# Kernel optimization log

Hardware: AMD Instinct MI355X
Metric: run time of the kernel (lower is better)

Reference implementation:

```python
import jax, jax.numpy as jnp
import numpy as np

N = 100000       # num_nodes
E = 800000       # num edges (avg degree 8)
EMB = 64         # emb_dim
HID = 256        # hidden_dim


def setup_inputs() -> dict:
    key = jax.random.key(0)
    k1, k2, k3, k4, k5, k6, k7 = jax.random.split(key, 7)
    def xavier(k, fan_in, fan_out):
        limit = float(np.sqrt(6.0 / (fan_in + fan_out)))
        return jax.random.uniform(k, (fan_in, fan_out), jnp.float32, -limit, limit)
    return {
        "row": jax.random.randint(k1, (E,), 0, N, dtype=jnp.int64) if jax.config.jax_enable_x64 else jax.random.randint(k1, (E,), 0, N).astype(jnp.int32),
        "col": jax.random.randint(k2, (E,), 0, N).astype(jnp.int32),
        "val": jax.random.uniform(k3, (E,), jnp.float32),
        "emb": jax.random.normal(k4, (N, EMB), jnp.float32) * 0.02,
        "W0": xavier(k5, EMB, HID),
        "W1": xavier(k6, HID, HID),
        "W2": xavier(k7, HID, HID),
    }


def reference(row, col, val, emb, W0, W1, W2):
    # SpMM: out[r] = sum_{edges e with row[e]==r} val[e] * emb[col[e]]
    msgs = val[:, None] * emb[col]                      # [E, EMB] gather + scale
    x = jax.ops.segment_sum(msgs, row, num_segments=N)  # [N, EMB] scatter-add
    # MLP (bias-free linears; dropout=0.0 / eval mode => identity)
    x = jax.nn.relu(x @ W0)   # [N, HID]
    x = jax.nn.relu(x @ W1)   # [N, HID]
    x = x @ W2                # [N, HID]
    return x
```

## Files before the change

kernel.cpp:

```cpp
#include <hip/hip_runtime.h>
#include <hip/hip_bf16.h>

#define EMB 64
#define HID 256

typedef __attribute__((ext_vector_type(8))) short short8_t;
typedef __attribute__((ext_vector_type(4))) float f32x4;

__device__ __forceinline__ unsigned short f2bf(float f)
{
    union { float f; unsigned int u; } c; c.f = f;
    unsigned int u = c.u;
    u += 0x7fffu + ((u >> 16) & 1u);
    return (unsigned short)(u >> 16);
}
__device__ __forceinline__ float bf2f(unsigned short b)
{
    union { unsigned int u; float f; } c; c.u = ((unsigned int)b) << 16;
    return c.f;
}

__global__ __launch_bounds__(256) void prep_kernel(
    const float* __restrict__ emb, const float* __restrict__ W0,
    const float* __restrict__ W1, const float* __restrict__ W2,
    int* __restrict__ counts, unsigned short* __restrict__ embb,
    unsigned short* __restrict__ W0f, unsigned short* __restrict__ W1f,
    unsigned short* __restrict__ W2f, int M, int zb, int cb)
{
    int b = blockIdx.x;
    if (b < zb) {
        int idx = (b * 256 + threadIdx.x) * 4;
        if (idx + 3 < M) {
            int4 z; z.x = 0; z.y = 0; z.z = 0; z.w = 0;
            *(int4*)&counts[idx] = z;
        } else {
            for (int i = idx; i < M; ++i) counts[i] = 0;
        }
        return;
    }
    b -= zb;
    if (b < cb) {
        int idx = (b * 256 + threadIdx.x) * 4;
        if (idx + 3 < M * EMB) {
            float4 v = *(const float4*)&emb[idx];
            ushort4 o;
            o.x = f2bf(v.x); o.y = f2bf(v.y); o.z = f2bf(v.z); o.w = f2bf(v.w);
            *(ushort4*)&embb[idx] = o;
        }
        return;
    }
    b -= cb;
    if (b < 8) {
        int i    = b * 256 + threadIdx.x;
        int lane = i & 63;
        int kc   = (i >> 6) & 1;
        int nt   = i >> 7;
        int lr   = lane & 15, kg = lane >> 4;
        unsigned short tmp[8];
#pragma unroll
        for (int j = 0; j < 8; ++j)
            tmp[j] = f2bf(W0[(kc * 32 + kg * 8 + j) * HID + nt * 16 + lr]);
        *(short8_t*)&W0f[(size_t)i * 8] = *(short8_t*)tmp;
        return;
    }
    b -= 8;
    if (b < 32) {
        int i    = b * 256 + threadIdx.x;
        int lane = i & 63;
        int kc   = (i >> 6) & 7;
        int nt   = i >> 9;
        int lr   = lane & 15, kg = lane >> 4;
        unsigned short tmp[8];
#pragma unroll
        for (int j = 0; j < 8; ++j)
            tmp[j] = f2bf(W1[(kc * 32 + kg * 8 + j) * HID + nt * 16 + lr]);
        *(short8_t*)&W1f[(size_t)i * 8] = *(short8_t*)tmp;
        return;
    }
    b -= 32;
    {
        int i    = b * 256 + threadIdx.x;
        int lane = i & 63;
        int kc   = (i >> 6) & 7;
        int nt   = i >> 9;
        int lr   = lane & 15, kg = lane >> 4;
        unsigned short tmp[8];
#pragma unroll
        for (int j = 0; j < 8; ++j)
            tmp[j] = f2bf(W2[(kc * 32 + kg * 8 + j) * HID + nt * 16 + lr]);
        *(short8_t*)&W2f[(size_t)i * 8] = *(short8_t*)tmp;
    }
}

__global__ __launch_bounds__(256) void hist_kernel(
    const int* __restrict__ row, int* __restrict__ counts, int E)
{
    int base = (blockIdx.x * 256 + threadIdx.x) * 4;
    if (base + 3 < E) {
        int4 r4 = *(const int4*)&row[base];
        atomicAdd(&counts[r4.x], 1);
        atomicAdd(&counts[r4.y], 1);
        atomicAdd(&counts[r4.z], 1);
        atomicAdd(&counts[r4.w], 1);
    } else {
        for (int i = base; i < E; ++i) atomicAdd(&counts[row[i]], 1);
    }
}

__global__ __launch_bounds__(256) void scan_phase1(
    const int* __restrict__ counts, int* __restrict__ excl,
    int* __restrict__ blockSums, int n)
{
    __shared__ int s[256];
    int t = threadIdx.x;
    int base = blockIdx.x * 1024 + t * 4;
    int4 v = {0, 0, 0, 0};
    if (base + 3 < n) {
        v = *(const int4*)&counts[base];
    } else {
        if (base + 0 < n) v.x = counts[base + 0];
        if (base + 1 < n) v.y = counts[base + 1];
        if (base + 2 < n) v.z = counts[base + 2];
        if (base + 3 < n) v.w = counts[base + 3];
    }
    int tsum = v.x + v.y + v.z + v.w;
    s[t] = tsum;
    __syncthreads();
#pragma unroll
    for (int off = 1; off < 256; off <<= 1) {
        int val = (t >= off) ? s[t - off] : 0;
        __syncthreads();
        s[t] += val;
        __syncthreads();
    }
    if (t == 255) blockSums[blockIdx.x] = s[255];
    int e0 = s[t] - tsum;
    int e1 = e0 + v.x;
    int e2 = e1 + v.y;
    int e3 = e2 + v.z;
    if (base + 0 < n) excl[base + 0] = e0;
    if (base + 1 < n) excl[base + 1] = e1;
    if (base + 2 < n) excl[base + 2] = e2;
    if (base + 3 < n) excl[base + 3] = e3;
}

__global__ __launch_bounds__(256) void scan_phase2(int* blockSums, int nb)
{
    __shared__ int s[256];
    int t = threadIdx.x;
    int v = (t < nb) ? blockSums[t] : 0;
    s[t] = v;
    __syncthreads();
#pragma unroll
    for (int off = 1; off < 256; off <<= 1) {
        int val = (t >= off) ? s[t - off] : 0;
        __syncthreads();
        s[t] += val;
        __syncthreads();
    }
    if (t < nb) blockSums[t] = s[t] - v;
}

__global__ __launch_bounds__(256) void scan_phase3(
    int* __restrict__ offsets, const int* __restrict__ blockSums,
    int* __restrict__ cursor, int n)
{
    int i = blockIdx.x * 256 + threadIdx.x;
    if (i >= n) return;
    int o = offsets[i] + blockSums[i >> 10];
    offsets[i] = o;
    cursor[i]  = o;
}

__global__ __launch_bounds__(256) void scatter_kernel(
    const int* __restrict__ row, const int* __restrict__ col,
    const float* __restrict__ val, int* __restrict__ cursor,
    uint2* __restrict__ edata, int E)
{
    int e = blockIdx.x * 256 + threadIdx.x;
    if (e >= E) return;
    int r = row[e];
    int pos = atomicAdd(&cursor[r], 1);
    uint2 d;
    d.x = (unsigned)col[e];
    d.y = __float_as_uint(val[e]);
    edata[pos] = d;
}

__global__ __launch_bounds__(256) void pull_kernel(
    const int* __restrict__ offsets, const int* __restrict__ counts,
    const uint2* __restrict__ edata, const unsigned short* __restrict__ embb,
    unsigned short* __restrict__ xb, int Nn)
{
    int r    = blockIdx.x * 4 + (threadIdx.x >> 6);
    int lane = threadIdx.x & 63;
    if (r >= Nn) return;
    int beg = offsets[r];
    int cnt = counts[r];
    float acc = 0.f;
    for (int i = 0; i < cnt; i += 8) {
        uint2 ed[8];
#pragma unroll
        for (int j = 0; j < 8; ++j) {
            int idx = i + j;
            idx = (idx < cnt) ? idx : (cnt - 1);
            ed[j] = edata[beg + idx];
        }
        float g[8];
#pragma unroll
        for (int j = 0; j < 8; ++j)
            g[j] = bf2f(embb[(size_t)ed[j].x * EMB + lane]);
#pragma unroll
        for (int j = 0; j < 8; ++j) {
            float v = (i + j < cnt) ? __uint_as_float(ed[j].y) : 0.f;
            acc += v * g[j];
        }
    }
    xb[(size_t)r * EMB + lane] = f2bf(acc);
}

__global__ __launch_bounds__(256) void mlp_fused(
    const unsigned short* __restrict__ xb,
    const unsigned short* __restrict__ W0f,
    const unsigned short* __restrict__ W1f,
    const unsigned short* __restrict__ W2f,
    float* __restrict__ out, int M)
{
    __shared__ unsigned short H[64 * 256];

    const int t    = threadIdx.x;
    const int lane = t & 63;
    const int w    = t >> 6;
    const int lr   = lane & 15;
    const int kg   = lane >> 4;
    const int row0 = blockIdx.x * 64;
    char* Hb = (char*)H;

#define HOFF(row, bytecol) ((((row) * 512) + (bytecol)) ^ (((row) & 7) << 4))

    short8_t ax[2][4];
#pragma unroll
    for (int kc = 0; kc < 2; ++kc)
#pragma unroll
        for (int m = 0; m < 4; ++m) {
            int gr = row0 + m * 16 + lr;
            ax[kc][m] = *(const short8_t*)(xb + (size_t)(gr < M ? gr : 0) * EMB
                                           + kc * 32 + kg * 8);
        }
    f32x4 acc[4][4] = {};
#pragma unroll
    for (int kc = 0; kc < 2; ++kc) {
        short8_t b[4];
#pragma unroll
        for (int n = 0; n < 4; ++n)
            b[n] = *(const short8_t*)&W0f[(size_t)(((w * 4 + n) * 2 + kc) * 64 + lane) * 8];
#pragma unroll
        for (int m = 0; m < 4; ++m)
#pragma unroll
            for (int n = 0; n < 4; ++n)
                acc[m][n] = __builtin_amdgcn_mfma_f32_16x16x32_bf16(
                    ax[kc][m], b[n], acc[m][n], 0, 0, 0);
    }
#pragma unroll
    for (int m = 0; m < 4; ++m)
#pragma unroll
        for (int r = 0; r < 4; ++r)
#pragma unroll
            for (int n = 0; n < 4; ++n)
                *(unsigned short*)(Hb + HOFF(m * 16 + kg * 4 + r,
                                             (w * 64 + n * 16 + lr) * 2)) =
                    f2bf(fmaxf(acc[m][n][r], 0.f));
    __syncthreads();

    f32x4 acc2[4][4] = {};
#pragma unroll
    for (int kc = 0; kc < 8; ++kc) {
        short8_t a[4], b[4];
#pragma unroll
        for (int n = 0; n < 4; ++n)
            b[n] = *(const short8_t*)&W1f[(size_t)(((w * 4 + n) * 8 + kc) * 64 + lane) * 8];
#pragma unroll
        for (int m = 0; m < 4; ++m)
            a[m] = *(const short8_t*)(Hb + HOFF(m * 16 + lr, kc * 64 + kg * 16));
#pragma unroll
        for (int m = 0; m < 4; ++m)
#pragma unroll
            for (int n = 0; n < 4; ++n)
                acc2[m][n] = __builtin_amdgcn_mfma_f32_16x16x32_bf16(
                    a[m], b[n], acc2[m][n], 0, 0, 0);
    }
    __syncthreads();
#pragma unroll
    for (int m = 0; m < 4; ++m)
#pragma unroll
        for (int r = 0; r < 4; ++r)
#pragma unroll
            for (int n = 0; n < 4; ++n)
                *(unsigned short*)(Hb + HOFF(m * 16 + kg * 4 + r,
                                             (w * 64 + n * 16 + lr) * 2)) =
                    f2bf(fmaxf(acc2[m][n][r], 0.f));
    __syncthreads();

    f32x4 acc3[4][4] = {};
#pragma unroll
    for (int kc = 0; kc < 8; ++kc) {
        short8_t a[4], b[4];
#pragma unroll
        for (int n = 0; n < 4; ++n)
            b[n] = *(const short8_t*)&W2f[(size_t)(((w * 4 + n) * 8 + kc) * 64 + lane) * 8];
#pragma unroll
        for (int m = 0; m < 4; ++m)
            a[m] = *(const short8_t*)(Hb + HOFF(m * 16 + lr, kc * 64 + kg * 16));
#pragma unroll
        for (int m = 0; m < 4; ++m)
#pragma unroll
            for (int n = 0; n < 4; ++n)
                acc3[m][n] = __builtin_amdgcn_mfma_f32_16x16x32_bf16(
                    a[m], b[n], acc3[m][n], 0, 0, 0);
    }
#pragma unroll
    for (int m = 0; m < 4; ++m)
#pragma unroll
        for (int r = 0; r < 4; ++r) {
            int gr = row0 + m * 16 + kg * 4 + r;
            if (gr < M)
#pragma unroll
                for (int n = 0; n < 4; ++n)
                    out[(size_t)gr * HID + w * 64 + n * 16 + lr] = acc3[m][n][r];
        }
#undef HOFF
}

__global__ __launch_bounds__(256) void spmm_kernel(
    const int* __restrict__ row, const int* __restrict__ col,
    const float* __restrict__ val, const float* __restrict__ emb,
    float* __restrict__ x, int E)
{
    int gid  = blockIdx.x * blockDim.x + threadIdx.x;
    int e    = gid >> 6;
    int lane = gid & 63;
    if (e >= E) return;
    unsafeAtomicAdd(&x[(size_t)row[e] * EMB + lane],
                    val[e] * emb[(size_t)col[e] * EMB + lane]);
}

template<int K, bool RELU>
__global__ __launch_bounds__(256) void gemm_f32(
    const float* A, const float* __restrict__ B, float* C, int M)
{
    __shared__ float As[64][17];
    __shared__ float Bs[16][256];

    const int t    = threadIdx.x;
    const int tn   = t & 15;
    const int row0 = blockIdx.x * 64;
    const int sk = t & 15;
    const int sm = (t >> 4) * 4;

    float acc[4][16];
#pragma unroll
    for (int i = 0; i < 4; ++i)
#pragma unroll
        for (int j = 0; j < 16; ++j) acc[i][j] = 0.f;

    const int mB = ((t & 63) >> 4) * 4;
    const int wq = t >> 6;
    const int myM = (wq * 16) + mB;

    for (int k0 = 0; k0 < K; k0 += 16) {
        __syncthreads();
#pragma unroll
        for (int i = 0; i < 4; ++i) {
            int m  = sm + i;
            int gr = row0 + m;
            As[m][sk] = (gr < M) ? A[(size_t)gr * K + k0 + sk] : 0.f;
        }
#pragma unroll
        for (int r = 0; r < 16; ++r)
            Bs[r][t] = B[(size_t)(k0 + r) * 256 + t];
        __syncthreads();

#pragma unroll
        for (int kk = 0; kk < 16; ++kk) {
            float a0 = As[myM + 0][kk];
            float a1 = As[myM + 1][kk];
            float a2 = As[myM + 2][kk];
            float a3 = As[myM + 3][kk];
            float4 b[4];
#pragma unroll
            for (int j = 0; j < 4; ++j)
                b[j] = *(const float4*)&Bs[kk][tn * 4 + j * 64];
#pragma unroll
            for (int j = 0; j < 4; ++j) {
                acc[0][j*4+0] += a0 * b[j].x;  acc[0][j*4+1] += a0 * b[j].y;
                acc[0][j*4+2] += a0 * b[j].z;  acc[0][j*4+3] += a0 * b[j].w;
                acc[1][j*4+0] += a1 * b[j].x;  acc[1][j*4+1] += a1 * b[j].y;
                acc[1][j*4+2] += a1 * b[j].z;  acc[1][j*4+3] += a1 * b[j].w;
                acc[2][j*4+0] += a2 * b[j].x;  acc[2][j*4+1] += a2 * b[j].y;
                acc[2][j*4+2] += a2 * b[j].z;  acc[2][j*4+3] += a2 * b[j].w;
                acc[3][j*4+0] += a3 * b[j].x;  acc[3][j*4+1] += a3 * b[j].y;
                acc[3][j*4+2] += a3 * b[j].z;  acc[3][j*4+3] += a3 * b[j].w;
            }
        }
    }

#pragma unroll
    for (int i = 0; i < 4; ++i) {
        int gr = row0 + myM + i;
        if (gr < M) {
#pragma unroll
            for (int j = 0; j < 4; ++j) {
                float4 o;
                o.x = acc[i][j*4+0]; o.y = acc[i][j*4+1];
                o.z = acc[i][j*4+2]; o.w = acc[i][j*4+3];
                if (RELU) {
                    o.x = fmaxf(o.x, 0.f); o.y = fmaxf(o.y, 0.f);
                    o.z = fmaxf(o.z, 0.f); o.w = fmaxf(o.w, 0.f);
                }
                *(float4*)&C[(size_t)gr * 256 + tn * 4 + j * 64] = o;
            }
        }
    }
}

extern "C" void kernel_launch(void* const* d_in, const int* in_sizes, int n_in,
                              void* d_out, int out_size, void* d_ws, size_t ws_size,
                              hipStream_t stream)
{
    const int*   row = (const int*)d_in[0];
    const int*   col = (const int*)d_in[1];
    const float* val = (const float*)d_in[2];
    const float* emb = (const float*)d_in[3];
    const float* W0  = (const float*)d_in[4];
    const float* W1  = (const float*)d_in[5];
    const float* W2  = (const float*)d_in[6];
    float* out = (float*)d_out;

    const int E = in_sizes[0];
    const int M = in_sizes[3] / EMB;

    char* ws = (char*)d_ws;

    size_t off = 0;
    auto alloc = [&](size_t bytes) { size_t o = off; off = (off + bytes + 255) & ~(size_t)255; return o; };
    const size_t off_counts = alloc((size_t)M * 4);
    const size_t off_offs   = alloc((size_t)M * 4);
    const size_t off_cursor = alloc((size_t)M * 4);
    const size_t off_bsums  = alloc(1024);
    const size_t off_edata  = alloc((size_t)E * 8);
    const size_t off_embb   = alloc((size_t)M * EMB * 2);
    const size_t off_xb     = alloc((size_t)M * EMB * 2);
    const size_t off_w0     = alloc((size_t)EMB * HID * 2);
    const size_t off_w1     = alloc((size_t)HID * HID * 2);
    const size_t off_w2     = alloc((size_t)HID * HID * 2);
    const size_t need       = off;

    int gblocks = (M + 63) / 64;

    if (ws_size >= need) {
        int*   counts = (int*)(ws + off_counts);
        int*   offs   = (int*)(ws + off_offs);
        int*   cursor = (int*)(ws + off_cursor);
        int*   bsums  = (int*)(ws + off_bsums);
        uint2* edata  = (uint2*)(ws + off_edata);
        unsigned short* embb = (unsigned short*)(ws + off_embb);
        unsigned short* xb  = (unsigned short*)(ws + off_xb);
        unsigned short* W0f = (unsigned short*)(ws + off_w0);
        unsigned short* W1f = (unsigned short*)(ws + off_w1);
        unsigned short* W2f = (unsigned short*)(ws + off_w2);

        int zb = (M / 4 + 255) / 256;
        int cb = ((M * EMB) / 4 + 255) / 256;
        int prep_blocks = zb + cb + 8 + 32 + 32;
        prep_kernel<<<prep_blocks, 256, 0, stream>>>(
            emb, W0, W1, W2, counts, embb, W0f, W1f, W2f, M, zb, cb);

        hist_kernel<<<(E / 4 + 255) / 256, 256, 0, stream>>>(row, counts, E);
        int nb = (M + 1023) / 1024;
        scan_phase1<<<nb, 256, 0, stream>>>(counts, offs, bsums, M);
        scan_phase2<<<1, 256, 0, stream>>>(bsums, nb);
        scan_phase3<<<(M + 255) / 256, 256, 0, stream>>>(offs, bsums, cursor, M);
        scatter_kernel<<<(E + 255) / 256, 256, 0, stream>>>(row, col, val, cursor, edata, E);

        pull_kernel<<<(M + 3) / 4, 256, 0, stream>>>(offs, counts, edata, embb, xb, M);

        mlp_fused<<<gblocks, 256, 0, stream>>>(xb, W0f, W1f, W2f, out, M);
    } else {
        float* x = (float*)ws;
        (void)hipMemsetAsync(x, 0, (size_t)M * EMB * sizeof(float), stream);
        spmm_kernel<<<(E + 3) / 4, 256, 0, stream>>>(row, col, val, emb, x, E);
        gemm_f32<EMB, true ><<<gblocks, 256, 0, stream>>>(x,   W0, out, M);
        gemm_f32<HID, true ><<<gblocks, 256, 0, stream>>>(out, W1, out, M);
        gemm_f32<HID, false><<<gblocks, 256, 0, stream>>>(out, W2, out, M);
    }
}
```

Baseline: 201.0 us.

## Vectorize scatter, grid-stride pull with prefetch, stage MLP output through LDS

```diff
diff --git a/kernel.cpp b/kernel.cpp
--- a/kernel.cpp
+++ b/kernel.cpp
@@ -177,46 +177,74 @@
     const float* __restrict__ val, int* __restrict__ cursor,
     uint2* __restrict__ edata, int E)
 {
-    int e = blockIdx.x * 256 + threadIdx.x;
-    if (e >= E) return;
-    int r = row[e];
-    int pos = atomicAdd(&cursor[r], 1);
-    uint2 d;
-    d.x = (unsigned)col[e];
-    d.y = __float_as_uint(val[e]);
-    edata[pos] = d;
-}
-
+    int base = (blockIdx.x * 256 + threadIdx.x) * 4;
+    if (base + 3 < E) {
+        int4   r4 = *(const int4*)&row[base];
+        int4   c4 = *(const int4*)&col[base];
+        float4 v4 = *(const float4*)&val[base];
+        int p0 = atomicAdd(&cursor[r4.x], 1);
+        int p1 = atomicAdd(&cursor[r4.y], 1);
+        int p2 = atomicAdd(&cursor[r4.z], 1);
+        int p3 = atomicAdd(&cursor[r4.w], 1);
+        uint2 d;
+        d.x = (unsigned)c4.x; d.y = __float_as_uint(v4.x); edata[p0] = d;
+        d.x = (unsigned)c4.y; d.y = __float_as_uint(v4.y); edata[p1] = d;
+        d.x = (unsigned)c4.z; d.y = __float_as_uint(v4.z); edata[p2] = d;
+        d.x = (unsigned)c4.w; d.y = __float_as_uint(v4.w); edata[p3] = d;
+    } else {
+        for (int e = base; e < E; ++e) {
+            int pos = atomicAdd(&cursor[row[e]], 1);
+            uint2 d;
+            d.x = (unsigned)col[e];
+            d.y = __float_as_uint(val[e]);
+            edata[pos] = d;
+        }
+    }
+}
+
+#define ROWS_PER_WAVE 8
 __global__ __launch_bounds__(256) void pull_kernel(
     const int* __restrict__ offsets, const int* __restrict__ counts,
     const uint2* __restrict__ edata, const unsigned short* __restrict__ embb,
     unsigned short* __restrict__ xb, int Nn)
 {
-    int r    = blockIdx.x * 4 + (threadIdx.x >> 6);
-    int lane = threadIdx.x & 63;
-    if (r >= Nn) return;
-    int beg = offsets[r];
-    int cnt = counts[r];
-    float acc = 0.f;
-    for (int i = 0; i < cnt; i += 8) {
-        uint2 ed[8];
-#pragma unroll
-        for (int j = 0; j < 8; ++j) {
-            int idx = i + j;
-            idx = (idx < cnt) ? idx : (cnt - 1);
-            ed[j] = edata[beg + idx];
-        }
-        float g[8];
-#pragma unroll
-        for (int j = 0; j < 8; ++j)
-            g[j] = bf2f(embb[(size_t)ed[j].x * EMB + lane]);
-#pragma unroll
-        for (int j = 0; j < 8; ++j) {
-            float v = (i + j < cnt) ? __uint_as_float(ed[j].y) : 0.f;
-            acc += v * g[j];
-        }
-    }
-    xb[(size_t)r * EMB + lane] = f2bf(acc);
+    const int nw   = gridDim.x * 4;
+    const int wid  = blockIdx.x * 4 + (threadIdx.x >> 6);
+    const int lane = threadIdx.x & 63;
+    if (wid >= Nn) return;
+
+    int beg = __builtin_amdgcn_readfirstlane(offsets[wid]);
+    int cnt = __builtin_amdgcn_readfirstlane(counts[wid]);
+    for (int r = wid; r < Nn; r += nw) {
+        int rn = r + nw;
+        int begN = 0, cntN = 0;
+        if (rn < Nn) {
+            begN = __builtin_amdgcn_readfirstlane(offsets[rn]);
+            cntN = __builtin_amdgcn_readfirstlane(counts[rn]);
+        }
+
+        float acc = 0.f;
+        for (int i = 0; i < cnt; i += 8) {
+            uint2 ed[8];
+#pragma unroll
+            for (int j = 0; j < 8; ++j) {
+                int idx = i + j;
+                idx = (idx < cnt) ? idx : (cnt - 1);
+                ed[j] = edata[beg + idx];
+            }
+            float g[8];
+#pragma unroll
+            for (int j = 0; j < 8; ++j)
+                g[j] = bf2f(embb[(size_t)ed[j].x * EMB + lane]);
+#pragma unroll
+            for (int j = 0; j < 8; ++j) {
+                float v = (i + j < cnt) ? __uint_as_float(ed[j].y) : 0.f;
+                acc += v * g[j];
+            }
+        }
+        xb[(size_t)r * EMB + lane] = f2bf(acc);
+        beg = begN; cnt = cntN;
+    }
 }
 
 __global__ __launch_bounds__(256) void mlp_fused(
@@ -318,16 +346,26 @@
                 acc3[m][n] = __builtin_amdgcn_mfma_f32_16x16x32_bf16(
                     a[m], b[n], acc3[m][n], 0, 0, 0);
     }
-#pragma unroll
-    for (int m = 0; m < 4; ++m)
-#pragma unroll
-        for (int r = 0; r < 4; ++r) {
-            int gr = row0 + m * 16 + kg * 4 + r;
+    __syncthreads();
+
+    float* Hf = (float*)H;
+    const int ebase = w * 1280;
+#pragma unroll
+    for (int m = 0; m < 4; ++m) {
+#pragma unroll
+        for (int n = 0; n < 4; ++n)
+#pragma unroll
+            for (int r = 0; r < 4; ++r)
+                Hf[ebase + (kg * 4 + r) * 68 + n * 16 + lr] = acc3[m][n][r];
+#pragma unroll
+        for (int p = 0; p < 4; ++p) {
+            int rl = (lane >> 4) + p * 4;
+            f32x4 v = *(const f32x4*)&Hf[ebase + rl * 68 + (lane & 15) * 4];
+            int gr = row0 + m * 16 + rl;
             if (gr < M)
-#pragma unroll
-                for (int n = 0; n < 4; ++n)
-                    out[(size_t)gr * HID + w * 64 + n * 16 + lr] = acc3[m][n][r];
-        }
+                *(f32x4*)&out[(size_t)gr * HID + w * 64 + (lane & 15) * 4] = v;
+        }
+    }
 #undef HOFF
 }
 
@@ -455,8 +493,6 @@
     const size_t off_w2     = alloc((size_t)HID * HID * 2);
     const size_t need       = off;
 
-    int gblocks = (M + 63) / 64;
-
     if (ws_size >= need) {
         int*   counts = (int*)(ws + off_counts);
         int*   offs   = (int*)(ws + off_offs);
@@ -480,15 +516,18 @@
         scan_phase1<<<nb, 256, 0, stream>>>(counts, offs, bsums, M);
         scan_phase2<<<1, 256, 0, stream>>>(bsums, nb);
         scan_phase3<<<(M + 255) / 256, 256, 0, stream>>>(offs, bsums, cursor, M);
-        scatter_kernel<<<(E + 255) / 256, 256, 0, stream>>>(row, col, val, cursor, edata, E);
-
-        pull_kernel<<<(M + 3) / 4, 256, 0, stream>>>(offs, counts, edata, embb, xb, M);
-
+        scatter_kernel<<<(E / 4 + 255) / 256, 256, 0, stream>>>(row, col, val, cursor, edata, E);
+
+        int pull_blocks = (M + 4 * ROWS_PER_WAVE - 1) / (4 * ROWS_PER_WAVE);
+        pull_kernel<<<pull_blocks, 256, 0, stream>>>(offs, counts, edata, embb, xb, M);
+
+        int gblocks = (M + 63) / 64;
         mlp_fused<<<gblocks, 256, 0, stream>>>(xb, W0f, W1f, W2f, out, M);
     } else {
         float* x = (float*)ws;
         (void)hipMemsetAsync(x, 0, (size_t)M * EMB * sizeof(float), stream);
         spmm_kernel<<<(E + 3) / 4, 256, 0, stream>>>(row, col, val, emb, x, E);
+        int gblocks = (M + 63) / 64;
         gemm_f32<EMB, true ><<<gblocks, 256, 0, stream>>>(x,   W0, out, M);
         gemm_f32<HID, true ><<<gblocks, 256, 0, stream>>>(out, W1, out, M);
         gemm_f32<HID, false><<<gblocks, 256, 0, stream>>>(out, W2, out, M);
```

New measurement: 218.7 us. 1.09x slower.
